# Kernel optimization log

Measured on AMD Instinct MI355X. Metric: run time of the kernel, lower is better.

The kernel has to match this reference:

```python
import jax, jax.numpy as jnp
import numpy as np

DIM_IN = 512
DIM_HEAD = 64
HEADS = 8
KV_HEADS = 2
CONTEXT_LEN = 4096
B, N = 4, 2048


def setup_inputs() -> dict:
    key = jax.random.key(0)
    ks = jax.random.split(key, 6)
    s = 1.0 / np.sqrt(DIM_IN)
    return {
        "x": jax.random.normal(ks[0], (B, DIM_IN, N), dtype=jnp.float32),
        "gamma": jnp.ones((DIM_IN,), jnp.float32),
        "beta": jnp.zeros((DIM_IN,), jnp.float32),
        "Wq": jax.random.normal(ks[1], (DIM_IN, DIM_HEAD * HEADS), jnp.float32) * s,
        "Wkv": jax.random.normal(ks[2], (DIM_IN, DIM_HEAD * KV_HEADS * 2), jnp.float32) * s,
        "Wout": jax.random.normal(ks[3], (DIM_HEAD * HEADS, DIM_IN), jnp.float32) * (1.0 / np.sqrt(DIM_HEAD * HEADS)),
        "bout": jnp.zeros((DIM_IN,), jnp.float32),
    }


def _rotate_half(t):
    t1, t2 = jnp.split(t, 2, axis=-1)
    return jnp.concatenate([-t2, t1], axis=-1)


def _xpos_rotary(q, k, n, dim_head, scale_base):
    # lucidrains-style xPos rotary embedding
    pos = jnp.arange(n, dtype=jnp.float32)
    inv_freq = 1.0 / (10000.0 ** (jnp.arange(0, dim_head, 2, dtype=jnp.float32) / dim_head))
    freqs = pos[:, None] * inv_freq[None, :]            # (n, dh/2)
    freqs = jnp.concatenate([freqs, freqs], axis=-1)    # (n, dh)
    base_scale = (jnp.arange(0, dim_head, 2, dtype=jnp.float32) + 0.4 * dim_head) / (1.4 * dim_head)
    power = (pos - n // 2) / scale_base                 # (n,)
    scale = base_scale[None, :] ** power[:, None]       # (n, dh/2)
    scale = jnp.concatenate([scale, scale], axis=-1)    # (n, dh)
    cos, sin = jnp.cos(freqs), jnp.sin(freqs)
    q = (q * cos + _rotate_half(q) * sin) * scale
    k = (k * cos + _rotate_half(k) * sin) / scale
    return q, k


def reference(x, gamma, beta, Wq, Wkv, Wout, bout):
    b, d, n = x.shape
    h, kvh, dh = HEADS, KV_HEADS, DIM_HEAD
    xt = jnp.swapaxes(x, 1, 2)                           # (b, n, d)
    mu = jnp.mean(xt, axis=-1, keepdims=True)
    var = jnp.mean((xt - mu) ** 2, axis=-1, keepdims=True)
    xn = (xt - mu) * jax.lax.rsqrt(var + 1e-5) * gamma + beta
    q = (xn @ Wq).reshape(b, n, h, dh).transpose(0, 2, 1, 3)      # (b, h, n, dh)
    kv = xn @ Wkv
    k, v = jnp.split(kv, 2, axis=-1)
    k = k.reshape(b, n, kvh, dh).transpose(0, 2, 1, 3)            # (b, kvh, n, dh)
    v = v.reshape(b, n, kvh, dh).transpose(0, 2, 1, 3)
    r = h // kvh
    # repeat 'b h n d -> b (r h) n d': tile whole kv-head block r times
    k = jnp.tile(k, (1, r, 1, 1))
    v = jnp.tile(v, (1, r, 1, 1))
    q, k = _xpos_rotary(q, k, n, dh, CONTEXT_LEN)
    scores = jnp.einsum("bhqd,bhkd->bhqk", q, k) * (1.0 / np.sqrt(dh))
    attn = jax.nn.softmax(scores, axis=-1)
    out = jnp.einsum("bhqk,bhkd->bhqd", attn, v)                  # (b, h, n, dh)
    out = out.transpose(0, 2, 1, 3).reshape(b, n, h * dh)
    y = xn + out @ Wout + bout                                    # residual uses normed x
    return jnp.swapaxes(y, 1, 2)                                  # (b, d, n)
```

## Files before the change

kernel.cpp:

```cpp
#include <hip/hip_runtime.h>
#include <stdint.h>

#define DIM 512
#define DH  64
#define NH  8
#define NKV 2
#define NB  4
#define NS  2048
#define TAB (NS*32)

typedef __attribute__((ext_vector_type(8))) short short8;
typedef __attribute__((ext_vector_type(4))) short s16x4;
typedef __attribute__((ext_vector_type(4))) float f32x4;
typedef __attribute__((ext_vector_type(16))) float f32x16;
typedef __attribute__((ext_vector_type(2))) unsigned uint2v;
typedef __attribute__((ext_vector_type(4))) unsigned uint4v;

__device__ __forceinline__ unsigned short f2bf(float f) {
  union { float f; unsigned u; } v; v.f = f;
  return (unsigned short)((v.u + 0x7fffu + ((v.u >> 16) & 1u)) >> 16);
}
__device__ __forceinline__ float bf2f(unsigned short b) {
  union { unsigned u; float f; } v; v.u = ((unsigned)b) << 16;
  return v.f;
}
__device__ __forceinline__ unsigned cvt_pk_bf16(float a, float b) {
  unsigned r;
  asm("v_cvt_pk_bf16_f32 %0, %1, %2" : "=v"(r) : "v"(a), "v"(b));
  return r;
}
__device__ __forceinline__ float exp2_raw(float x) {
  float r;
  asm("v_exp_f32 %0, %1" : "=v"(r) : "v"(x));
  return r;
}

__global__ __launch_bounds__(256) void ln_kernel(const float* __restrict__ x,
    const float* __restrict__ gamma, const float* __restrict__ beta,
    unsigned short* __restrict__ xn) {
  const int b = blockIdx.y;
  const int n0 = blockIdx.x * 32;
  const int tid = threadIdx.x;
  const int nl = tid & 31, grp = tid >> 5;
  const float* xb = x + (size_t)b * DIM * NS + (size_t)grp * 64 * NS + n0 + nl;
  float v[64];
  float s = 0.f, s2 = 0.f;
  #pragma unroll
  for (int i = 0; i < 64; ++i) {
    v[i] = xb[(size_t)i * NS];
    s += v[i]; s2 += v[i] * v[i];
  }
  __shared__ float sm[8][32], sq[8][32], mu_s[32], rs_s[32];
  sm[grp][nl] = s; sq[grp][nl] = s2;
  __syncthreads();
  if (tid < 32) {
    float ts = 0.f, ts2 = 0.f;
    #pragma unroll
    for (int g = 0; g < 8; ++g) { ts += sm[g][tid]; ts2 += sq[g][tid]; }
    float mu = ts * (1.f/512.f);
    float var = ts2 * (1.f/512.f) - mu*mu;
    mu_s[tid] = mu; rs_s[tid] = rsqrtf(var + 1e-5f);
  }
  __syncthreads();
  const float mu = mu_s[nl], rs = rs_s[nl];
  unsigned short* dst = &xn[((size_t)(b*NS + n0 + nl))*DIM + grp*64];
  #pragma unroll
  for (int c = 0; c < 8; ++c) {
    short8 o;
    #pragma unroll
    for (int j = 0; j < 8; ++j) {
      int d = grp*64 + c*8 + j;
      o[j] = (short)f2bf((v[c*8 + j] - mu) * rs * gamma[d] + beta[d]);
    }
    *(short8*)&dst[c*8] = o;
  }
}

__global__ __launch_bounds__(256) void prep_kernel(const float* __restrict__ Wq,
    const float* __restrict__ Wkv, const float* __restrict__ Wout,
    unsigned short* __restrict__ Wqkvt, unsigned short* __restrict__ Woutt,
    float* __restrict__ tabs) {
  __shared__ float t[64][65];
  const int id = blockIdx.x;
  const int tid = threadIdx.x;
  if (id >= 160) {
    int base = (id - 160) * 256 + tid;
    #pragma unroll 4
    for (int ii = 0; ii < 32; ++ii) {
      int tix = base + ii * 2048;
      int pos = tix >> 5, i = tix & 31;
      float inv = exp2f(-(float)i * (13.287712379549449f / 32.f));
      float ang = (float)pos * inv;
      float sv, cv; sincosf(ang, &sv, &cv);
      float bse = ((float)(2*i) + 25.6f) / 89.6f;
      float power = ((float)pos - 1024.f) / 4096.f;
      float sc = exp2f(power * log2f(bse));
      tabs[tix]         = cv;
      tabs[TAB + tix]   = sv;
      tabs[2*TAB + tix] = sc * 0.125f * 1.4426950408889634f;
      tabs[3*TAB + tix] = 1.f / sc;
    }
    return;
  }
  const float* src; int W, k0, c0; unsigned short* dst; int drow0;
  if (id < 64)      { src = Wq;  W = 512; k0 = (id>>3)*64;        c0 = (id&7)*64;        dst = Wqkvt; drow0 = c0; }
  else if (id < 96) { int i2 = id-64; src = Wkv; W = 256; k0 = (i2>>2)*64; c0 = (i2&3)*64; dst = Wqkvt; drow0 = 512 + c0; }
  else              { int i3 = id-96; src = Wout; W = 512; k0 = (i3>>3)*64; c0 = (i3&7)*64; dst = Woutt; drow0 = c0; }
  #pragma unroll 4
  for (int it = 0; it < 16; ++it) {
    int row = it*4 + (tid>>6), col = tid & 63;
    t[row][col] = src[(size_t)(k0+row)*W + c0 + col];
  }
  __syncthreads();
  #pragma unroll 4
  for (int it = 0; it < 16; ++it) {
    int row = it*4 + (tid>>6), col = tid & 63;
    dst[(size_t)(drow0 + row)*512 + k0 + col] = f2bf(t[col][row]);
  }
}

__global__ __launch_bounds__(256, 3) void qkv_kernel(const unsigned short* __restrict__ A,
    const unsigned short* __restrict__ Bt, const float* __restrict__ tabs,
    unsigned short* __restrict__ q, unsigned short* __restrict__ k,
    unsigned short* __restrict__ v) {
  __shared__ __align__(16) short As[2][64][40];
  __shared__ __align__(16) short Bs[2][128][40];
  const int m0 = blockIdx.x * 64, ntile = blockIdx.y, n0 = ntile * 128;
  const int tid = threadIdx.x, w = tid >> 6, lane = tid & 63;
  const int wr = w >> 1, wc = w & 1;
  f32x4 acc[2][4];
  #pragma unroll
  for (int i = 0; i < 2; ++i)
    #pragma unroll
    for (int j = 0; j < 4; ++j) acc[i][j] = (f32x4){0.f,0.f,0.f,0.f};
  const int rA = tid >> 2, c8 = (tid & 3) * 8;
  const unsigned short* Ar0 = &A[(size_t)(m0 + rA)*DIM + c8];
  const unsigned short* Br0 = &Bt[(size_t)(n0 + rA)*DIM + c8];
  const unsigned short* Br1 = &Bt[(size_t)(n0 + 64 + rA)*DIM + c8];
  *(short8*)&As[0][rA][c8]      = *(const short8*)Ar0;
  *(short8*)&Bs[0][rA][c8]      = *(const short8*)Br0;
  *(short8*)&Bs[0][64 + rA][c8] = *(const short8*)Br1;
  short8 pa0 = *(const short8*)(Ar0 + 32);
  short8 pb0 = *(const short8*)(Br0 + 32);
  short8 pb1 = *(const short8*)(Br1 + 32);
  __syncthreads();
  for (int t = 0; t < 16; ++t) {
    const int cur = t & 1;
    short8 af[2], bfr[4];
    #pragma unroll
    for (int mf = 0; mf < 2; ++mf)
      af[mf] = *(const short8*)&As[cur][wr*32 + mf*16 + (lane & 15)][(lane >> 4)*8];
    #pragma unroll
    for (int nf = 0; nf < 4; ++nf)
      bfr[nf] = *(const short8*)&Bs[cur][wc*64 + nf*16 + (lane & 15)][(lane >> 4)*8];
    __builtin_amdgcn_s_setprio(1);
    #pragma unroll
    for (int mf = 0; mf < 2; ++mf)
      #pragma unroll
      for (int nf = 0; nf < 4; ++nf)
        acc[mf][nf] = __builtin_amdgcn_mfma_f32_16x16x32_bf16(af[mf], bfr[nf], acc[mf][nf], 0, 0, 0);
    __builtin_amdgcn_s_setprio(0);
    if (t < 15) {
      *(short8*)&As[cur^1][rA][c8]      = pa0;
      *(short8*)&Bs[cur^1][rA][c8]      = pb0;
      *(short8*)&Bs[cur^1][64 + rA][c8] = pb1;
      if (t < 14) {
        const int kc = (t + 2) * 32;
        pa0 = *(const short8*)(Ar0 + kc);
        pb0 = *(const short8*)(Br0 + kc);
        pb1 = *(const short8*)(Br1 + kc);
      }
      __syncthreads();
    }
  }
  const int mw = m0 + wr*32, cw = n0 + wc*64;
  if (ntile < 4) {
    #pragma unroll
    for (int nfp = 0; nfp < 2; ++nfp) {
      const int c_lo = cw + nfp*16 + (lane & 15);
      const int head = c_lo >> 6, ii = c_lo & 31;
      const float* tb = tabs + ii;
      #pragma unroll
      for (int mf = 0; mf < 2; ++mf) {
        #pragma unroll
        for (int r = 0; r < 4; ++r) {
          int mm = mw + mf*16 + (lane >> 4)*4 + r;
          int bb = mm >> 11, n = mm & (NS-1);
          float cv = tb[n*32], sv = tb[TAB + n*32], qs = tb[2*TAB + n*32];
          float lo = acc[mf][nfp][r], hi = acc[mf][nfp+2][r];
          size_t base = (((size_t)bb*NH + head)*NS + n)*DH;
          q[base + ii]      = f2bf((lo*cv - hi*sv)*qs);
          q[base + ii + 32] = f2bf((hi*cv + lo*sv)*qs);
        }
      }
    }
  } else if (ntile == 4) {
    #pragma unroll
    for (int nfp = 0; nfp < 2; ++nfp) {
      const int c_lo = cw + nfp*16 + (lane & 15);
      const int kvh = (c_lo - 512) >> 6, ii = c_lo & 31;
      const float* tb = tabs + ii;
      #pragma unroll
      for (int mf = 0; mf < 2; ++mf) {
        #pragma unroll
        for (int r = 0; r < 4; ++r) {
          int mm = mw + mf*16 + (lane >> 4)*4 + r;
          int bb = mm >> 11, n = mm & (NS-1);
          float cv = tb[n*32], sv = tb[TAB + n*32], ks = tb[3*TAB + n*32];
          float lo = acc[mf][nfp][r], hi = acc[mf][nfp+2][r];
          size_t base = (((size_t)bb*NKV + kvh)*NS + n)*DH;
          k[base + ii]      = f2bf((lo*cv - hi*sv)*ks);
          k[base + ii + 32] = f2bf((hi*cv + lo*sv)*ks);
        }
      }
    }
  } else {
    #pragma unroll
    for (int nf = 0; nf < 4; ++nf) {
      const int c = cw + nf*16 + (lane & 15);
      const int rel = c - 640;
      const int kvh = rel >> 6, dd = rel & 63;
      #pragma unroll
      for (int mf = 0; mf < 2; ++mf) {
        int mm = mw + mf*16 + (lane >> 4)*4;
        int bb = mm >> 11, n = mm & (NS-1);
        s16x4 sv4;
        #pragma unroll
        for (int r = 0; r < 4; ++r) sv4[r] = (short)f2bf(acc[mf][nf][r]);
        *(s16x4*)&v[(((size_t)bb*NKV + kvh)*DH + dd)*NS + n] = sv4;
      }
    }
  }
}

__global__ __launch_bounds__(256, 2) void attn_kernel(const unsigned short* __restrict__ q,
    const unsigned short* __restrict__ kg, const unsigned short* __restrict__ vtp,
    unsigned short* __restrict__ ao) {
  __shared__ __align__(16) short kt[2][64][72];
  __shared__ __align__(16) short vt[2][64][72];
  __shared__ float l_lds[4][32];
  const int bid = blockIdx.x;
  const int dsr = (bid & 7) * 64 + (bid >> 3);
  const int qt = dsr & 15, bh = dsr >> 4;
  const int h = bh & 7, b = bh >> 3;
  const int kvh = h & (NKV-1);
  const int q0 = qt * 128;
  const int tid = threadIdx.x, w = tid >> 6, lane = tid & 63;
  const int l31 = lane & 31, hf = lane >> 5;
  short8 q8[4];
  const unsigned short* qp = q + (((size_t)b*NH + h)*NS + q0 + w*32 + l31)*DH + hf*8;
  #pragma unroll
  for (int s = 0; s < 4; ++s) q8[s] = *(const short8*)(qp + s*16);
  const unsigned short* kb = kg + ((size_t)b*NKV + kvh)*NS*DH;
  const unsigned short* vb = vtp + ((size_t)b*NKV + kvh)*DH*NS;
  const int srow = tid >> 2, scol = (tid & 3) * 16;
  *(short8*)&kt[0][srow][scol]     = *(const short8*)&kb[(size_t)srow*DH + scol];
  *(short8*)&kt[0][srow][scol + 8] = *(const short8*)&kb[(size_t)srow*DH + scol + 8];
  *(short8*)&vt[0][srow][scol]     = *(const short8*)&vb[(size_t)srow*NS + scol];
  *(short8*)&vt[0][srow][scol + 8] = *(const short8*)&vb[(size_t)srow*NS + scol + 8];
  short8 kr0 = *(const short8*)&kb[(size_t)(64 + srow)*DH + scol];
  short8 kr1 = *(const short8*)&kb[(size_t)(64 + srow)*DH + scol + 8];
  short8 vr0 = *(const short8*)&vb[(size_t)srow*NS + 64 + scol];
  short8 vr1 = *(const short8*)&vb[(size_t)srow*NS + 64 + scol + 8];
  f32x16 o0 = {}, o1 = {};
  float lsum = 0.f;
  __syncthreads();
  for (int t = 0; t < 32; ++t) {
    const int cur = t & 1;
    short8 kf0[4], kf1[4];
    #pragma unroll
    for (int s = 0; s < 4; ++s) {
      kf0[s] = *(const short8*)&kt[cur][l31][s*16 + hf*8];
      kf1[s] = *(const short8*)&kt[cur][32 + l31][s*16 + hf*8];
    }
    f32x16 st0 = {}, st1 = {};
    __builtin_amdgcn_s_setprio(1);
    #pragma unroll
    for (int s = 0; s < 4; ++s) {
      st0 = __builtin_amdgcn_mfma_f32_32x32x16_bf16(kf0[s], q8[s], st0, 0, 0, 0);
      st1 = __builtin_amdgcn_mfma_f32_32x32x16_bf16(kf1[s], q8[s], st1, 0, 0, 0);
    }
    __builtin_amdgcn_s_setprio(0);
    float p0[16], p1[16];
    #pragma unroll
    for (int r = 0; r < 16; ++r) {
      p0[r] = exp2_raw(st0[r]);
      p1[r] = exp2_raw(st1[r]);
      lsum += p0[r] + p1[r];
    }
    short8 paf[4];
    #pragma unroll
    for (int t2 = 0; t2 < 2; ++t2) {
      const float* pp = t2 ? p1 : p0;
      #pragma unroll
      for (int w16 = 0; w16 < 2; ++w16) {
        const int rb = w16*8;
        unsigned x = cvt_pk_bf16(pp[rb+0], pp[rb+1]);
        unsigned z = cvt_pk_bf16(pp[rb+2], pp[rb+3]);
        unsigned y = cvt_pk_bf16(pp[rb+4], pp[rb+5]);
        unsigned u = cvt_pk_bf16(pp[rb+6], pp[rb+7]);
        uint2v r1 = __builtin_amdgcn_permlane32_swap(x, y, false, false);
        uint2v r2 = __builtin_amdgcn_permlane32_swap(z, u, false, false);
        uint4v pk4;
        pk4[0] = r1[0]; pk4[1] = r2[0]; pk4[2] = r1[1]; pk4[3] = r2[1];
        paf[t2*2 + w16] = __builtin_bit_cast(short8, pk4);
      }
    }
    __builtin_amdgcn_s_setprio(1);
    #pragma unroll
    for (int kwin = 0; kwin < 4; ++kwin) {
      short8 vf0 = *(const short8*)&vt[cur][l31][kwin*16 + hf*8];
      short8 vf1 = *(const short8*)&vt[cur][32 + l31][kwin*16 + hf*8];
      o0 = __builtin_amdgcn_mfma_f32_32x32x16_bf16(paf[kwin], vf0, o0, 0, 0, 0);
      o1 = __builtin_amdgcn_mfma_f32_32x32x16_bf16(paf[kwin], vf1, o1, 0, 0, 0);
    }
    __builtin_amdgcn_s_setprio(0);
    if (t < 31) {
      *(short8*)&kt[cur^1][srow][scol]     = kr0;
      *(short8*)&kt[cur^1][srow][scol + 8] = kr1;
      *(short8*)&vt[cur^1][srow][scol]     = vr0;
      *(short8*)&vt[cur^1][srow][scol + 8] = vr1;
      if (t < 30) {
        const int k2 = (t + 2) * 64;
        kr0 = *(const short8*)&kb[(size_t)(k2 + srow)*DH + scol];
        kr1 = *(const short8*)&kb[(size_t)(k2 + srow)*DH + scol + 8];
        vr0 = *(const short8*)&vb[(size_t)srow*NS + k2 + scol];
        vr1 = *(const short8*)&vb[(size_t)srow*NS + k2 + scol + 8];
      }
      __syncthreads();
    }
  }
  lsum += __shfl_xor(lsum, 32);
  if (hf == 0) {
    float rl;
    asm("v_rcp_f32 %0, %1" : "=v"(rl) : "v"(lsum));
    l_lds[w][l31] = rl;
  }
  asm volatile("s_waitcnt lgkmcnt(0)" ::: "memory");
  __builtin_amdgcn_sched_barrier(0);
  #pragma unroll
  for (int r = 0; r < 16; ++r) {
    const int ql = (r & 3) + 8*(r >> 2) + 4*hf;
    const float rl = l_lds[w][ql];
    const int n = q0 + w*32 + ql;
    unsigned short* aor = &ao[((size_t)b*NS + n)*DIM + h*DH + l31];
    aor[0]  = f2bf(o0[r] * rl);
    aor[32] = f2bf(o1[r] * rl);
  }
}

__global__ __launch_bounds__(256, 3) void out_kernel(const unsigned short* __restrict__ A,
    const unsigned short* __restrict__ Bt, const unsigned short* __restrict__ xn,
    const float* __restrict__ bout, float* __restrict__ out) {
  __shared__ __align__(16) short As[2][64][40];
  __shared__ __align__(16) short Bs[2][128][40];
  const int m0 = blockIdx.x * 64, n0 = blockIdx.y * 128;
  const int tid = threadIdx.x, w = tid >> 6, lane = tid & 63;
  const int wr = w >> 1, wc = w & 1;
  f32x4 acc[2][4];
  #pragma unroll
  for (int i = 0; i < 2; ++i)
    #pragma unroll
    for (int j = 0; j < 4; ++j) acc[i][j] = (f32x4){0.f,0.f,0.f,0.f};
  const int rA = tid >> 2, c8 = (tid & 3) * 8;
  const unsigned short* Ar0 = &A[(size_t)(m0 + rA)*DIM + c8];
  const unsigned short* Br0 = &Bt[(size_t)(n0 + rA)*DIM + c8];
  const unsigned short* Br1 = &Bt[(size_t)(n0 + 64 + rA)*DIM + c8];
  *(short8*)&As[0][rA][c8]      = *(const short8*)Ar0;
  *(short8*)&Bs[0][rA][c8]      = *(const short8*)Br0;
  *(short8*)&Bs[0][64 + rA][c8] = *(const short8*)Br1;
  short8 pa0 = *(const short8*)(Ar0 + 32);
  short8 pb0 = *(const short8*)(Br0 + 32);
  short8 pb1 = *(const short8*)(Br1 + 32);
  __syncthreads();
  for (int t = 0; t < 16; ++t) {
    const int cur = t & 1;
    short8 af[2], bfr[4];
    #pragma unroll
    for (int mf = 0; mf < 2; ++mf)
      af[mf] = *(const short8*)&As[cur][wr*32 + mf*16 + (lane & 15)][(lane >> 4)*8];
    #pragma unroll
    for (int nf = 0; nf < 4; ++nf)
      bfr[nf] = *(const short8*)&Bs[cur][wc*64 + nf*16 + (lane & 15)][(lane >> 4)*8];
    __builtin_amdgcn_s_setprio(1);
    #pragma unroll
    for (int mf = 0; mf < 2; ++mf)
      #pragma unroll
      for (int nf = 0; nf < 4; ++nf)
        acc[mf][nf] = __builtin_amdgcn_mfma_f32_16x16x32_bf16(af[mf], bfr[nf], acc[mf][nf], 0, 0, 0);
    __builtin_amdgcn_s_setprio(0);
    if (t < 15) {
      *(short8*)&As[cur^1][rA][c8]      = pa0;
      *(short8*)&Bs[cur^1][rA][c8]      = pb0;
      *(short8*)&Bs[cur^1][64 + rA][c8] = pb1;
      if (t < 14) {
        const int kc = (t + 2) * 32;
        pa0 = *(const short8*)(Ar0 + kc);
        pb0 = *(const short8*)(Br0 + kc);
        pb1 = *(const short8*)(Br1 + kc);
      }
      __syncthreads();
    }
  }
  const int mw = m0 + wr*32, cw = n0 + wc*64;
  #pragma unroll
  for (int nf = 0; nf < 4; ++nf) {
    const int d = cw + nf*16 + (lane & 15);
    const float bo = bout[d];
    #pragma unroll
    for (int mf = 0; mf < 2; ++mf) {
      const int mb = mw + mf*16 + (lane >> 4)*4;
      const int bb = mb >> 11, n = mb & (NS-1);
      f32x4 res;
      #pragma unroll
      for (int r = 0; r < 4; ++r)
        res[r] = acc[mf][nf][r] + bf2f(xn[(size_t)(mb + r)*DIM + d]) + bo;
      *(f32x4*)&out[((size_t)bb*DIM + d)*NS + n] = res;
    }
  }
}

extern "C" void kernel_launch(void* const* d_in, const int* in_sizes, int n_in,
                              void* d_out, int out_size, void* d_ws, size_t ws_size,
                              hipStream_t stream) {
  (void)in_sizes; (void)n_in; (void)out_size; (void)ws_size;
  const float* x     = (const float*)d_in[0];
  const float* gamma = (const float*)d_in[1];
  const float* beta  = (const float*)d_in[2];
  const float* Wq    = (const float*)d_in[3];
  const float* Wkv   = (const float*)d_in[4];
  const float* Wout  = (const float*)d_in[5];
  const float* bout  = (const float*)d_in[6];
  float* out = (float*)d_out;
  char* ws = (char*)d_ws;
  unsigned short* xn    = (unsigned short*)(ws);
  unsigned short* qb    = (unsigned short*)(ws + (size_t)(8<<20));
  unsigned short* kb    = (unsigned short*)(ws + (size_t)(16<<20));
  unsigned short* vb    = (unsigned short*)(ws + (size_t)(18<<20));
  unsigned short* ao    = (unsigned short*)(ws + (size_t)(20<<20));
  unsigned short* wqkvt = (unsigned short*)(ws + (size_t)(28<<20));
  unsigned short* woutt = (unsigned short*)(ws + (size_t)(28<<20) + 786432);
  float* tabs           = (float*)(ws + (size_t)(28<<20) + 786432 + 524288);

  ln_kernel<<<dim3(64, 4), dim3(256), 0, stream>>>(x, gamma, beta, xn);
  prep_kernel<<<dim3(168), dim3(256), 0, stream>>>(Wq, Wkv, Wout, wqkvt, woutt, tabs);
  qkv_kernel<<<dim3(128, 6), dim3(256), 0, stream>>>(xn, wqkvt, tabs, qb, kb, vb);
  attn_kernel<<<dim3(512), dim3(256), 0, stream>>>(qb, kb, vb, ao);
  out_kernel<<<dim3(128, 4), dim3(256), 0, stream>>>(ao, woutt, xn, bout, out);
}
```

Baseline: 90.29 us.

## Software-pipeline attention loop: overlap QK^T of next tile with softmax/PV of previous

```diff
diff --git a/kernel.cpp b/kernel.cpp
--- a/kernel.cpp
+++ b/kernel.cpp
@@ -256,13 +256,12 @@
   const int srow = tid >> 2, scol = (tid & 3) * 16;
   *(short8*)&kt[0][srow][scol]     = *(const short8*)&kb[(size_t)srow*DH + scol];
   *(short8*)&kt[0][srow][scol + 8] = *(const short8*)&kb[(size_t)srow*DH + scol + 8];
-  *(short8*)&vt[0][srow][scol]     = *(const short8*)&vb[(size_t)srow*NS + scol];
-  *(short8*)&vt[0][srow][scol + 8] = *(const short8*)&vb[(size_t)srow*NS + scol + 8];
   short8 kr0 = *(const short8*)&kb[(size_t)(64 + srow)*DH + scol];
   short8 kr1 = *(const short8*)&kb[(size_t)(64 + srow)*DH + scol + 8];
-  short8 vr0 = *(const short8*)&vb[(size_t)srow*NS + 64 + scol];
-  short8 vr1 = *(const short8*)&vb[(size_t)srow*NS + 64 + scol + 8];
+  short8 vr0 = *(const short8*)&vb[(size_t)srow*NS + scol];
+  short8 vr1 = *(const short8*)&vb[(size_t)srow*NS + scol + 8];
   f32x16 o0 = {}, o1 = {};
+  f32x16 st0_o = {}, st1_o = {};
   float lsum = 0.f;
   __syncthreads();
   for (int t = 0; t < 32; ++t) {
@@ -274,18 +273,72 @@
       kf1[s] = *(const short8*)&kt[cur][32 + l31][s*16 + hf*8];
     }
     f32x16 st0 = {}, st1 = {};
-    __builtin_amdgcn_s_setprio(1);
     #pragma unroll
     for (int s = 0; s < 4; ++s) {
       st0 = __builtin_amdgcn_mfma_f32_32x32x16_bf16(kf0[s], q8[s], st0, 0, 0, 0);
       st1 = __builtin_amdgcn_mfma_f32_32x32x16_bf16(kf1[s], q8[s], st1, 0, 0, 0);
     }
-    __builtin_amdgcn_s_setprio(0);
+    if (t > 0) {
+      float p0[16], p1[16];
+      #pragma unroll
+      for (int r = 0; r < 16; ++r) {
+        p0[r] = exp2_raw(st0_o[r]);
+        p1[r] = exp2_raw(st1_o[r]);
+        lsum += p0[r] + p1[r];
+      }
+      short8 paf[4];
+      #pragma unroll
+      for (int t2 = 0; t2 < 2; ++t2) {
+        const float* pp = t2 ? p1 : p0;
+        #pragma unroll
+        for (int w16 = 0; w16 < 2; ++w16) {
+          const int rb = w16*8;
+          unsigned x = cvt_pk_bf16(pp[rb+0], pp[rb+1]);
+          unsigned z = cvt_pk_bf16(pp[rb+2], pp[rb+3]);
+          unsigned y = cvt_pk_bf16(pp[rb+4], pp[rb+5]);
+          unsigned u = cvt_pk_bf16(pp[rb+6], pp[rb+7]);
+          uint2v r1 = __builtin_amdgcn_permlane32_swap(x, y, false, false);
+          uint2v r2 = __builtin_amdgcn_permlane32_swap(z, u, false, false);
+          uint4v pk4;
+          pk4[0] = r1[0]; pk4[1] = r2[0]; pk4[2] = r1[1]; pk4[3] = r2[1];
+          paf[t2*2 + w16] = __builtin_bit_cast(short8, pk4);
+        }
+      }
+      __builtin_amdgcn_s_setprio(1);
+      #pragma unroll
+      for (int kwin = 0; kwin < 4; ++kwin) {
+        short8 vf0 = *(const short8*)&vt[cur^1][l31][kwin*16 + hf*8];
+        short8 vf1 = *(const short8*)&vt[cur^1][32 + l31][kwin*16 + hf*8];
+        o0 = __builtin_amdgcn_mfma_f32_32x32x16_bf16(paf[kwin], vf0, o0, 0, 0, 0);
+        o1 = __builtin_amdgcn_mfma_f32_32x32x16_bf16(paf[kwin], vf1, o1, 0, 0, 0);
+      }
+      __builtin_amdgcn_s_setprio(0);
+    }
+    if (t < 31) {
+      *(short8*)&kt[cur^1][srow][scol]     = kr0;
+      *(short8*)&kt[cur^1][srow][scol + 8] = kr1;
+    }
+    *(short8*)&vt[cur][srow][scol]     = vr0;
+    *(short8*)&vt[cur][srow][scol + 8] = vr1;
+    if (t < 30) {
+      const int k2 = (t + 2) * 64;
+      kr0 = *(const short8*)&kb[(size_t)(k2 + srow)*DH + scol];
+      kr1 = *(const short8*)&kb[(size_t)(k2 + srow)*DH + scol + 8];
+    }
+    if (t < 31) {
+      const int kv1 = (t + 1) * 64;
+      vr0 = *(const short8*)&vb[(size_t)srow*NS + kv1 + scol];
+      vr1 = *(const short8*)&vb[(size_t)srow*NS + kv1 + scol + 8];
+    }
+    __syncthreads();
+    st0_o = st0; st1_o = st1;
+  }
+  {
     float p0[16], p1[16];
     #pragma unroll
     for (int r = 0; r < 16; ++r) {
-      p0[r] = exp2_raw(st0[r]);
-      p1[r] = exp2_raw(st1[r]);
+      p0[r] = exp2_raw(st0_o[r]);
+      p1[r] = exp2_raw(st1_o[r]);
       lsum += p0[r] + p1[r];
     }
     short8 paf[4];
@@ -306,28 +359,12 @@
         paf[t2*2 + w16] = __builtin_bit_cast(short8, pk4);
       }
     }
-    __builtin_amdgcn_s_setprio(1);
     #pragma unroll
     for (int kwin = 0; kwin < 4; ++kwin) {
-      short8 vf0 = *(const short8*)&vt[cur][l31][kwin*16 + hf*8];
-      short8 vf1 = *(const short8*)&vt[cur][32 + l31][kwin*16 + hf*8];
+      short8 vf0 = *(const short8*)&vt[1][l31][kwin*16 + hf*8];
+      short8 vf1 = *(const short8*)&vt[1][32 + l31][kwin*16 + hf*8];
       o0 = __builtin_amdgcn_mfma_f32_32x32x16_bf16(paf[kwin], vf0, o0, 0, 0, 0);
       o1 = __builtin_amdgcn_mfma_f32_32x32x16_bf16(paf[kwin], vf1, o1, 0, 0, 0);
-    }
-    __builtin_amdgcn_s_setprio(0);
-    if (t < 31) {
-      *(short8*)&kt[cur^1][srow][scol]     = kr0;
-      *(short8*)&kt[cur^1][srow][scol + 8] = kr1;
-      *(short8*)&vt[cur^1][srow][scol]     = vr0;
-      *(short8*)&vt[cur^1][srow][scol + 8] = vr1;
-      if (t < 30) {
-        const int k2 = (t + 2) * 64;
-        kr0 = *(const short8*)&kb[(size_t)(k2 + srow)*DH + scol];
-        kr1 = *(const short8*)&kb[(size_t)(k2 + srow)*DH + scol + 8];
-        vr0 = *(const short8*)&vb[(size_t)srow*NS + k2 + scol];
-        vr1 = *(const short8*)&vb[(size_t)srow*NS + k2 + scol + 8];
-      }
-      __syncthreads();
     }
   }
   lsum += __shfl_xor(lsum, 32);
```

New measurement: 91.79 us. No clear change (+1.7%).

## Split attention over key halves, merge partials in out-projection, fuse LN with prep

Applied to the files above, without the earlier changes.

```diff
diff --git a/kernel.cpp b/kernel.cpp
--- a/kernel.cpp
+++ b/kernel.cpp
@@ -34,55 +34,72 @@
   asm("v_exp_f32 %0, %1" : "=v"(r) : "v"(x));
   return r;
 }
-
-__global__ __launch_bounds__(256) void ln_kernel(const float* __restrict__ x,
+__device__ __forceinline__ float rcp_raw(float x) {
+  float r;
+  asm("v_rcp_f32 %0, %1" : "=v"(r) : "v"(x));
+  return r;
+}
+__device__ __forceinline__ short8 merge8(short8 a, short8 b, float rl) {
+  uint4v u;
+  #pragma unroll
+  for (int i = 0; i < 4; ++i) {
+    float x0 = (bf2f((unsigned short)a[2*i])   + bf2f((unsigned short)b[2*i]))   * rl;
+    float x1 = (bf2f((unsigned short)a[2*i+1]) + bf2f((unsigned short)b[2*i+1])) * rl;
+    u[i] = cvt_pk_bf16(x0, x1);
+  }
+  return __builtin_bit_cast(short8, u);
+}
+
+__global__ __launch_bounds__(256) void lnprep_kernel(const float* __restrict__ x,
     const float* __restrict__ gamma, const float* __restrict__ beta,
-    unsigned short* __restrict__ xn) {
-  const int b = blockIdx.y;
-  const int n0 = blockIdx.x * 32;
+    const float* __restrict__ Wq, const float* __restrict__ Wkv, const float* __restrict__ Wout,
+    unsigned short* __restrict__ xn, unsigned short* __restrict__ Wqkvt,
+    unsigned short* __restrict__ Woutt, float* __restrict__ tabs) {
+  __shared__ float t[64][65];
+  const int gid = blockIdx.x;
   const int tid = threadIdx.x;
-  const int nl = tid & 31, grp = tid >> 5;
-  const float* xb = x + (size_t)b * DIM * NS + (size_t)grp * 64 * NS + n0 + nl;
-  float v[64];
-  float s = 0.f, s2 = 0.f;
-  #pragma unroll
-  for (int i = 0; i < 64; ++i) {
-    v[i] = xb[(size_t)i * NS];
-    s += v[i]; s2 += v[i] * v[i];
-  }
-  __shared__ float sm[8][32], sq[8][32], mu_s[32], rs_s[32];
-  sm[grp][nl] = s; sq[grp][nl] = s2;
-  __syncthreads();
-  if (tid < 32) {
-    float ts = 0.f, ts2 = 0.f;
-    #pragma unroll
-    for (int g = 0; g < 8; ++g) { ts += sm[g][tid]; ts2 += sq[g][tid]; }
-    float mu = ts * (1.f/512.f);
-    float var = ts2 * (1.f/512.f) - mu*mu;
-    mu_s[tid] = mu; rs_s[tid] = rsqrtf(var + 1e-5f);
-  }
-  __syncthreads();
-  const float mu = mu_s[nl], rs = rs_s[nl];
-  unsigned short* dst = &xn[((size_t)(b*NS + n0 + nl))*DIM + grp*64];
-  #pragma unroll
-  for (int c = 0; c < 8; ++c) {
-    short8 o;
-    #pragma unroll
-    for (int j = 0; j < 8; ++j) {
-      int d = grp*64 + c*8 + j;
-      o[j] = (short)f2bf((v[c*8 + j] - mu) * rs * gamma[d] + beta[d]);
-    }
-    *(short8*)&dst[c*8] = o;
-  }
-}
-
-__global__ __launch_bounds__(256) void prep_kernel(const float* __restrict__ Wq,
-    const float* __restrict__ Wkv, const float* __restrict__ Wout,
-    unsigned short* __restrict__ Wqkvt, unsigned short* __restrict__ Woutt,
-    float* __restrict__ tabs) {
-  __shared__ float t[64][65];
-  const int id = blockIdx.x;
-  const int tid = threadIdx.x;
+  if (gid < 256) {
+    const int b = gid >> 6;
+    const int n0 = (gid & 63) * 32;
+    const int nl = tid & 31, grp = tid >> 5;
+    const float* xb = x + (size_t)b * DIM * NS + (size_t)grp * 64 * NS + n0 + nl;
+    float v[64];
+    float s = 0.f, s2 = 0.f;
+    #pragma unroll
+    for (int i = 0; i < 64; ++i) {
+      v[i] = xb[(size_t)i * NS];
+      s += v[i]; s2 += v[i] * v[i];
+    }
+    float* sm = &t[0][0];
+    float* sq = &t[8][0];
+    float* mu_s = &t[16][0];
+    float* rs_s = &t[17][0];
+    sm[grp*32 + nl] = s; sq[grp*32 + nl] = s2;
+    __syncthreads();
+    if (tid < 32) {
+      float ts = 0.f, ts2 = 0.f;
+      #pragma unroll
+      for (int g = 0; g < 8; ++g) { ts += sm[g*32 + tid]; ts2 += sq[g*32 + tid]; }
+      float mu = ts * (1.f/512.f);
+      float var = ts2 * (1.f/512.f) - mu*mu;
+      mu_s[tid] = mu; rs_s[tid] = rsqrtf(var + 1e-5f);
+    }
+    __syncthreads();
+    const float mu = mu_s[nl], rs = rs_s[nl];
+    unsigned short* dst = &xn[((size_t)(b*NS + n0 + nl))*DIM + grp*64];
+    #pragma unroll
+    for (int c = 0; c < 8; ++c) {
+      short8 o;
+      #pragma unroll
+      for (int j = 0; j < 8; ++j) {
+        int d = grp*64 + c*8 + j;
+        o[j] = (short)f2bf((v[c*8 + j] - mu) * rs * gamma[d] + beta[d]);
+      }
+      *(short8*)&dst[c*8] = o;
+    }
+    return;
+  }
+  const int id = gid - 256;
   if (id >= 160) {
     int base = (id - 160) * 256 + tid;
     #pragma unroll 4
@@ -233,15 +250,17 @@
   }
 }
 
-__global__ __launch_bounds__(256, 2) void attn_kernel(const unsigned short* __restrict__ q,
+__global__ __launch_bounds__(256, 4) void attn_kernel(const unsigned short* __restrict__ q,
     const unsigned short* __restrict__ kg, const unsigned short* __restrict__ vtp,
-    unsigned short* __restrict__ ao) {
+    unsigned short* __restrict__ op0, unsigned short* __restrict__ op1,
+    float* __restrict__ lp) {
   __shared__ __align__(16) short kt[2][64][72];
   __shared__ __align__(16) short vt[2][64][72];
-  __shared__ float l_lds[4][32];
   const int bid = blockIdx.x;
-  const int dsr = (bid & 7) * 64 + (bid >> 3);
-  const int qt = dsr & 15, bh = dsr >> 4;
+  const int dsr = (bid & 7) * 128 + (bid >> 3);
+  const int qt   = dsr & 15;
+  const int half = (dsr >> 4) & 1;
+  const int bh   = dsr >> 5;
   const int h = bh & 7, b = bh >> 3;
   const int kvh = h & (NKV-1);
   const int q0 = qt * 128;
@@ -253,19 +272,20 @@
   for (int s = 0; s < 4; ++s) q8[s] = *(const short8*)(qp + s*16);
   const unsigned short* kb = kg + ((size_t)b*NKV + kvh)*NS*DH;
   const unsigned short* vb = vtp + ((size_t)b*NKV + kvh)*DH*NS;
+  const int kbase = half * 1024;
   const int srow = tid >> 2, scol = (tid & 3) * 16;
-  *(short8*)&kt[0][srow][scol]     = *(const short8*)&kb[(size_t)srow*DH + scol];
-  *(short8*)&kt[0][srow][scol + 8] = *(const short8*)&kb[(size_t)srow*DH + scol + 8];
-  *(short8*)&vt[0][srow][scol]     = *(const short8*)&vb[(size_t)srow*NS + scol];
-  *(short8*)&vt[0][srow][scol + 8] = *(const short8*)&vb[(size_t)srow*NS + scol + 8];
-  short8 kr0 = *(const short8*)&kb[(size_t)(64 + srow)*DH + scol];
-  short8 kr1 = *(const short8*)&kb[(size_t)(64 + srow)*DH + scol + 8];
-  short8 vr0 = *(const short8*)&vb[(size_t)srow*NS + 64 + scol];
-  short8 vr1 = *(const short8*)&vb[(size_t)srow*NS + 64 + scol + 8];
+  *(short8*)&kt[0][srow][scol]     = *(const short8*)&kb[(size_t)(kbase + srow)*DH + scol];
+  *(short8*)&kt[0][srow][scol + 8] = *(const short8*)&kb[(size_t)(kbase + srow)*DH + scol + 8];
+  *(short8*)&vt[0][srow][scol]     = *(const short8*)&vb[(size_t)srow*NS + kbase + scol];
+  *(short8*)&vt[0][srow][scol + 8] = *(const short8*)&vb[(size_t)srow*NS + kbase + scol + 8];
+  short8 kr0 = *(const short8*)&kb[(size_t)(kbase + 64 + srow)*DH + scol];
+  short8 kr1 = *(const short8*)&kb[(size_t)(kbase + 64 + srow)*DH + scol + 8];
+  short8 vr0 = *(const short8*)&vb[(size_t)srow*NS + kbase + 64 + scol];
+  short8 vr1 = *(const short8*)&vb[(size_t)srow*NS + kbase + 64 + scol + 8];
   f32x16 o0 = {}, o1 = {};
   float lsum = 0.f;
   __syncthreads();
-  for (int t = 0; t < 32; ++t) {
+  for (int t = 0; t < 16; ++t) {
     const int cur = t & 1;
     short8 kf0[4], kf1[4];
     #pragma unroll
@@ -315,13 +335,13 @@
       o1 = __builtin_amdgcn_mfma_f32_32x32x16_bf16(paf[kwin], vf1, o1, 0, 0, 0);
     }
     __builtin_amdgcn_s_setprio(0);
-    if (t < 31) {
+    if (t < 15) {
       *(short8*)&kt[cur^1][srow][scol]     = kr0;
       *(short8*)&kt[cur^1][srow][scol + 8] = kr1;
       *(short8*)&vt[cur^1][srow][scol]     = vr0;
       *(short8*)&vt[cur^1][srow][scol + 8] = vr1;
-      if (t < 30) {
-        const int k2 = (t + 2) * 64;
+      if (t < 14) {
+        const int k2 = kbase + (t + 2) * 64;
         kr0 = *(const short8*)&kb[(size_t)(k2 + srow)*DH + scol];
         kr1 = *(const short8*)&kb[(size_t)(k2 + srow)*DH + scol + 8];
         vr0 = *(const short8*)&vb[(size_t)srow*NS + k2 + scol];
@@ -331,25 +351,21 @@
     }
   }
   lsum += __shfl_xor(lsum, 32);
-  if (hf == 0) {
-    float rl;
-    asm("v_rcp_f32 %0, %1" : "=v"(rl) : "v"(lsum));
-    l_lds[w][l31] = rl;
-  }
-  asm volatile("s_waitcnt lgkmcnt(0)" ::: "memory");
-  __builtin_amdgcn_sched_barrier(0);
+  if (hf == 0)
+    lp[(size_t)half*NB*NH*NS + ((size_t)b*NH + h)*NS + q0 + w*32 + l31] = lsum;
+  unsigned short* op = half ? op1 : op0;
   #pragma unroll
   for (int r = 0; r < 16; ++r) {
     const int ql = (r & 3) + 8*(r >> 2) + 4*hf;
-    const float rl = l_lds[w][ql];
     const int n = q0 + w*32 + ql;
-    unsigned short* aor = &ao[((size_t)b*NS + n)*DIM + h*DH + l31];
-    aor[0]  = f2bf(o0[r] * rl);
-    aor[32] = f2bf(o1[r] * rl);
-  }
-}
-
-__global__ __launch_bounds__(256, 3) void out_kernel(const unsigned short* __restrict__ A,
+    unsigned short* aor = &op[((size_t)b*NS + n)*DIM + h*DH + l31];
+    aor[0]  = f2bf(o0[r]);
+    aor[32] = f2bf(o1[r]);
+  }
+}
+
+__global__ __launch_bounds__(256, 3) void out_kernel(const unsigned short* __restrict__ op0,
+    const unsigned short* __restrict__ op1, const float* __restrict__ lp,
     const unsigned short* __restrict__ Bt, const unsigned short* __restrict__ xn,
     const float* __restrict__ bout, float* __restrict__ out) {
   __shared__ __align__(16) short As[2][64][40];
@@ -363,13 +379,21 @@
     #pragma unroll
     for (int j = 0; j < 4; ++j) acc[i][j] = (f32x4){0.f,0.f,0.f,0.f};
   const int rA = tid >> 2, c8 = (tid & 3) * 8;
-  const unsigned short* Ar0 = &A[(size_t)(m0 + rA)*DIM + c8];
+  const int rowm = m0 + rA;
+  const int b0 = rowm >> 11, nn0 = rowm & (NS-1);
+  const float* lp0 = lp + ((size_t)b0*NH)*NS + nn0;
+  const float* lp1 = lp0 + (size_t)NB*NH*NS;
+  const unsigned short* A0 = &op0[(size_t)rowm*DIM + c8];
+  const unsigned short* A1 = &op1[(size_t)rowm*DIM + c8];
   const unsigned short* Br0 = &Bt[(size_t)(n0 + rA)*DIM + c8];
   const unsigned short* Br1 = &Bt[(size_t)(n0 + 64 + rA)*DIM + c8];
-  *(short8*)&As[0][rA][c8]      = *(const short8*)Ar0;
+  float rlc = rcp_raw(lp0[0] + lp1[0]);
+  *(short8*)&As[0][rA][c8]      = merge8(*(const short8*)A0, *(const short8*)A1, rlc);
   *(short8*)&Bs[0][rA][c8]      = *(const short8*)Br0;
   *(short8*)&Bs[0][64 + rA][c8] = *(const short8*)Br1;
-  short8 pa0 = *(const short8*)(Ar0 + 32);
+  short8 pa0 = *(const short8*)(A0 + 32);
+  short8 pa1 = *(const short8*)(A1 + 32);
+  float rlp = rlc;
   short8 pb0 = *(const short8*)(Br0 + 32);
   short8 pb1 = *(const short8*)(Br1 + 32);
   __syncthreads();
@@ -390,14 +414,17 @@
         acc[mf][nf] = __builtin_amdgcn_mfma_f32_16x16x32_bf16(af[mf], bfr[nf], acc[mf][nf], 0, 0, 0);
     __builtin_amdgcn_s_setprio(0);
     if (t < 15) {
-      *(short8*)&As[cur^1][rA][c8]      = pa0;
+      *(short8*)&As[cur^1][rA][c8]      = merge8(pa0, pa1, rlp);
       *(short8*)&Bs[cur^1][rA][c8]      = pb0;
       *(short8*)&Bs[cur^1][64 + rA][c8] = pb1;
       if (t < 14) {
         const int kc = (t + 2) * 32;
-        pa0 = *(const short8*)(Ar0 + kc);
+        pa0 = *(const short8*)(A0 + kc);
+        pa1 = *(const short8*)(A1 + kc);
         pb0 = *(const short8*)(Br0 + kc);
         pb1 = *(const short8*)(Br1 + kc);
+        const int h2 = (t + 2) >> 1;
+        rlp = rcp_raw(lp0[h2*NS] + lp1[h2*NS]);
       }
       __syncthreads();
     }
@@ -437,14 +464,16 @@
   unsigned short* qb    = (unsigned short*)(ws + (size_t)(8<<20));
   unsigned short* kb    = (unsigned short*)(ws + (size_t)(16<<20));
   unsigned short* vb    = (unsigned short*)(ws + (size_t)(18<<20));
-  unsigned short* ao    = (unsigned short*)(ws + (size_t)(20<<20));
-  unsigned short* wqkvt = (unsigned short*)(ws + (size_t)(28<<20));
-  unsigned short* woutt = (unsigned short*)(ws + (size_t)(28<<20) + 786432);
-  float* tabs           = (float*)(ws + (size_t)(28<<20) + 786432 + 524288);
-
-  ln_kernel<<<dim3(64, 4), dim3(256), 0, stream>>>(x, gamma, beta, xn);
-  prep_kernel<<<dim3(168), dim3(256), 0, stream>>>(Wq, Wkv, Wout, wqkvt, woutt, tabs);
+  unsigned short* op0   = (unsigned short*)(ws + (size_t)(20<<20));
+  unsigned short* op1   = (unsigned short*)(ws + (size_t)(28<<20));
+  unsigned short* wqkvt = (unsigned short*)(ws + (size_t)(36<<20));
+  unsigned short* woutt = (unsigned short*)(ws + (size_t)(36<<20) + 786432);
+  float* tabs           = (float*)(ws + (size_t)(36<<20) + 786432 + 524288);
+  float* lp             = (float*)(ws + (size_t)(36<<20) + 786432 + 524288 + 1048576);
+
+  lnprep_kernel<<<dim3(424), dim3(256), 0, stream>>>(x, gamma, beta, Wq, Wkv, Wout,
+                                                     xn, wqkvt, woutt, tabs);
   qkv_kernel<<<dim3(128, 6), dim3(256), 0, stream>>>(xn, wqkvt, tabs, qb, kb, vb);
-  attn_kernel<<<dim3(512), dim3(256), 0, stream>>>(qb, kb, vb, ao);
-  out_kernel<<<dim3(128, 4), dim3(256), 0, stream>>>(ao, woutt, xn, bout, out);
-}
+  attn_kernel<<<dim3(1024), dim3(256), 0, stream>>>(qb, kb, vb, op0, op1, lp);
+  out_kernel<<<dim3(128, 4), dim3(256), 0, stream>>>(op0, op1, lp, woutt, xn, bout, out);
+}
```

After: 89.48 us. About the same (-0.9%).
